# Performance work log

Measured on AMD Instinct MI355X. Metric: run time of the kernel, lower is better.

The kernel has to match this reference:

```python
import jax, jax.numpy as jnp
import numpy as np

NEG_INF = -9e15  # matches torch's -9000000000000000.0 mask value
LEAKY_SLOPE = 0.2  # init alpha


def setup_inputs() -> dict:
    key = jax.random.key(0)
    k1, k2, k3, k4 = jax.random.split(key, 4)
    N, dim = 4096, 128
    hidden = jax.random.normal(k1, (N, dim), dtype=jnp.float32)
    adj = jax.random.randint(k2, (N, N), 0, 5)  # relation codes 0..4
    W = jax.random.normal(k3, (4, dim), dtype=jnp.float32) * (1.0 / np.sqrt(dim))
    b = jax.random.normal(k4, (4,), dtype=jnp.float32) * 0.01
    return {"hidden": hidden, "adj": adj, "W": W, "b": b}


def reference(hidden, adj, W, b):
    # e_k[i,j] = leakyrelu(sum_d h[i,d]*h[j,d]*W[k,d] + b[k])
    # equivalent to the torch repeat/view outer-product + four dim->1 Linears,
    # computed without materializing the [N,N,dim] intermediate.
    hw = hidden[None, :, :] * W[:, None, :]               # [4, N, dim]
    e = jnp.einsum('knd,md->knm', hw, hidden) + b[:, None, None]  # [4, N, N]
    e = jax.nn.leaky_relu(e, negative_slope=LEAKY_SLOPE)
    neg = jnp.asarray(NEG_INF, dtype=e.dtype)
    alpha = jnp.where(adj == 1, e[0], neg)
    alpha = jnp.where(adj == 2, e[1], alpha)
    alpha = jnp.where(adj == 3, e[2], alpha)
    alpha = jnp.where(adj == 4, e[3], alpha)
    alpha = jax.nn.softmax(alpha, axis=-1)                # [N, N]
    return alpha @ hidden                                  # [N, dim]
```

## Files before the change

### kernel.cpp

```cpp
#include <hip/hip_runtime.h>

#define NN 4096
#define DIM 128
#define TN 32
#define TM 64
#define NSPLIT 4
#define NTILES 16

typedef __attribute__((ext_vector_type(8))) short bf16x8;
typedef __attribute__((ext_vector_type(4))) float f32x4;

#define HRS 136
#define HCS 72
#define HROW_USH (TM * HRS)
#define HCOL_USH (128 * HCS)
#define TILE_USH (HROW_USH + HCOL_USH)
#define TILE_CHUNKS 35
#define PST 72

__device__ inline unsigned short f2bf(float x) {
    union { float f; unsigned u; } v; v.f = x;
    unsigned r = v.u + 0x7FFFu + ((v.u >> 16) & 1u);
    return (unsigned short)(r >> 16);
}

__device__ inline void dma16(const void* g, void* l) {
    __builtin_amdgcn_global_load_lds(
        (const __attribute__((address_space(1))) void*)g,
        (__attribute__((address_space(3))) void*)l,
        16, 0, 0);
}

__global__ __launch_bounds__(256) void prep_pack_kernel(
    const float* __restrict__ hidden,
    unsigned short* __restrict__ Hpack)
{
    __shared__ unsigned short T[16][HCS];
    const int tid = threadIdx.x;
    const int t0  = blockIdx.x >> 3;
    const int s   = blockIdx.x & 7;
    const int m0  = t0 * TM;
    unsigned short* rowdst = Hpack + (size_t)t0 * TILE_USH;
    unsigned short* coldst = rowdst + HROW_USH;

    {
        int row = tid >> 5;
        int c4  = (tid & 31) * 4;
        float4 v = *(const float4*)(hidden + (size_t)(m0 + 8 * s + row) * DIM + c4);
        ushort4 o;
        o.x = f2bf(v.x); o.y = f2bf(v.y); o.z = f2bf(v.z); o.w = f2bf(v.w);
        *(ushort4*)(rowdst + (8 * s + row) * HRS + c4) = o;
    }
    {
        int m  = tid >> 2;
        int dc = (tid & 3) * 4;
        float4 v = *(const float4*)(hidden + (size_t)(m0 + m) * DIM + 16 * s + dc);
        T[dc + 0][m] = f2bf(v.x);
        T[dc + 1][m] = f2bf(v.y);
        T[dc + 2][m] = f2bf(v.z);
        T[dc + 3][m] = f2bf(v.w);
    }
    __syncthreads();
    if (tid < 128) {
        int d  = tid >> 3;
        int c8 = (tid & 7) * 8;
        uint4 v = *(const uint4*)(&T[d][c8]);
        *(uint4*)(coldst + (16 * s + d) * HCS + c8) = v;
    }
}

__global__ __launch_bounds__(512)
__attribute__((amdgpu_waves_per_eu(4, 4)))
void gat_flash_kernel(
    const float* __restrict__ hidden,
    const unsigned short* __restrict__ Hpack,
    const int*   __restrict__ adj,
    const float* __restrict__ W,
    const float* __restrict__ bvec,
    float*       __restrict__ Opart,
    float*       __restrict__ lpart)
{
    __shared__ __align__(16) unsigned short HH[2][TILE_USH];
    __shared__ __align__(16) unsigned short Plc[TN * PST];
    __shared__ float redsum[8][16];

    const int tid  = threadIdx.x;
    const int w    = tid >> 6;
    const int lane = tid & 63;
    const int g    = lane >> 4;
    const int l15  = lane & 15;
    const int blk  = blockIdx.x;
    const int nbr  = blk >> 2;
    const int q4   = blk & 3;
    const int n0   = nbr * TN;
    const int gt0  = q4 * NTILES;
    const int rg   = w >> 2;
    const int msw  = w & 3;
    const int lofs = lane * 16;

    const float b0 = bvec[0], b1 = bvec[1], b2 = bvec[2], b3 = bvec[3];

    {
        const char* src = (const char*)(Hpack + (size_t)gt0 * TILE_USH);
        char* dst = (char*)&HH[0][0];
        #pragma unroll
        for (int it = 0; it < 5; ++it) {
            int chunk = it * 8 + w;
            if (chunk < TILE_CHUNKS)
                dma16(src + chunk * 1024 + lofs, dst + chunk * 1024);
        }
    }
    {
        #pragma unroll
        for (int it = 0; it < 2; ++it) {
            int idx = tid + 512 * it;
            int row = idx >> 3;
            int c16 = (idx & 7) * 16;
            int k = row >> 5, r = row & 31;
            const float* hrow = hidden + (size_t)(n0 + r) * DIM + c16;
            const float* wrow = W + k * DIM + c16;
            unsigned short* qdst = &HH[1][row * HRS + c16];
            #pragma unroll
            for (int c = 0; c < 4; ++c) {
                float4 hv = *(const float4*)(hrow + 4 * c);
                float4 wv = *(const float4*)(wrow + 4 * c);
                ushort4 o;
                o.x = f2bf(hv.x * wv.x); o.y = f2bf(hv.y * wv.y);
                o.z = f2bf(hv.z * wv.z); o.w = f2bf(hv.w * wv.w);
                *(ushort4*)(qdst + 4 * c) = o;
            }
        }
    }
    __syncthreads();

    bf16x8 Af[4][4];
    #pragma unroll
    for (int k = 0; k < 4; ++k)
        #pragma unroll
        for (int ks = 0; ks < 4; ++ks)
            Af[k][ks] = *(const bf16x8*)&HH[1][(k * 32 + rg * 16 + l15) * HRS + ks * 32 + 8 * g];
    __syncthreads();

    float lrow[4] = {0.f, 0.f, 0.f, 0.f};
    f32x4 Oacc[2];
    #pragma unroll
    for (int dt = 0; dt < 2; ++dt) Oacc[dt] = (f32x4){0.f, 0.f, 0.f, 0.f};

    const size_t arow = (size_t)(n0 + rg * 16 + 4 * g) * NN;
    int avc[4], avn[4];
    #pragma unroll
    for (int t = 0; t < 4; ++t)
        avc[t] = adj[arow + (size_t)t * NN + gt0 * TM + msw * 16 + l15];

    for (int tile = 0; tile < NTILES; ++tile) {
        const int cur = tile & 1;
        const int nxt = cur ^ 1;

        if (tile + 1 < NTILES) {
            const char* src = (const char*)(Hpack + (size_t)(gt0 + tile + 1) * TILE_USH);
            char* dst = (char*)&HH[nxt][0];
            #pragma unroll
            for (int it = 0; it < 5; ++it) {
                int chunk = it * 8 + w;
                if (chunk < TILE_CHUNKS)
                    dma16(src + chunk * 1024 + lofs, dst + chunk * 1024);
            }
        }

        f32x4 S[4];
        #pragma unroll
        for (int k = 0; k < 4; ++k) S[k] = (f32x4){0.f, 0.f, 0.f, 0.f};
        #pragma unroll
        for (int ks = 0; ks < 4; ++ks) {
            bf16x8 B = *(const bf16x8*)&HH[cur][(msw * 16 + l15) * HRS + ks * 32 + 8 * g];
            #pragma unroll
            for (int k = 0; k < 4; ++k)
                S[k] = __builtin_amdgcn_mfma_f32_16x16x32_bf16(Af[k][ks], B, S[k], 0, 0, 0);
        }

        #pragma unroll
        for (int t = 0; t < 4; ++t) {
            int a = avc[t];
            float s = S[0][t] + b0;
            s = (a == 2) ? S[1][t] + b1 : s;
            s = (a == 3) ? S[2][t] + b2 : s;
            s = (a == 4) ? S[3][t] + b3 : s;
            float e = fmaxf(s, 0.2f * s);
            float p = __expf(e);
            p = (a == 0) ? 0.f : p;
            lrow[t] += p;
            Plc[(rg * 16 + 4 * g + t) * PST + msw * 16 + l15] = f2bf(p);
        }

        if (tile + 1 < NTILES) {
            #pragma unroll
            for (int t = 0; t < 4; ++t)
                avn[t] = adj[arow + (size_t)t * NN + (size_t)(gt0 + tile + 1) * TM + msw * 16 + l15];
        }

        asm volatile("s_waitcnt lgkmcnt(0)\n\ts_barrier" ::: "memory");

        #pragma unroll
        for (int kc = 0; kc < 2; ++kc) {
            bf16x8 Pa = *(const bf16x8*)&Plc[(rg * 16 + l15) * PST + kc * 32 + 8 * g];
            #pragma unroll
            for (int dt = 0; dt < 2; ++dt) {
                bf16x8 Bv = *(const bf16x8*)&HH[cur][HROW_USH + (msw * 32 + dt * 16 + l15) * HCS + kc * 32 + 8 * g];
                Oacc[dt] = __builtin_amdgcn_mfma_f32_16x16x32_bf16(Pa, Bv, Oacc[dt], 0, 0, 0);
            }
        }

        #pragma unroll
        for (int i = 0; i < 4; ++i) avc[i] = avn[i];
        __syncthreads();
    }

    #pragma unroll
    for (int t = 0; t < 4; ++t) {
        float v = lrow[t];
        v += __shfl_xor(v, 1); v += __shfl_xor(v, 2);
        v += __shfl_xor(v, 4); v += __shfl_xor(v, 8);
        if (l15 == 0) redsum[w][4 * g + t] = v;
    }
    __syncthreads();
    if (tid < TN) {
        int rg2 = tid >> 4, rr = tid & 15;
        lpart[blk * TN + tid] = redsum[rg2 * 4 + 0][rr] + redsum[rg2 * 4 + 1][rr]
                              + redsum[rg2 * 4 + 2][rr] + redsum[rg2 * 4 + 3][rr];
    }
    float* Ob = Opart + (size_t)blk * (TN * DIM);
    #pragma unroll
    for (int dt = 0; dt < 2; ++dt)
        #pragma unroll
        for (int t = 0; t < 4; ++t)
            Ob[(rg * 16 + 4 * g + t) * DIM + msw * 32 + dt * 16 + l15] = Oacc[dt][t];
}

__global__ __launch_bounds__(256) void combine_kernel(
    const float* __restrict__ Opart, const float* __restrict__ lpart,
    float* __restrict__ out)
{
    int idx = blockIdx.x * 256 + threadIdx.x;
    int r = idx >> 7, d = idx & 127;
    int nbr = r >> 5, rr = r & 31;
    float O = 0.f, l = 0.f;
    #pragma unroll
    for (int q = 0; q < NSPLIT; ++q) {
        O += Opart[(size_t)(nbr * NSPLIT + q) * (TN * DIM) + rr * 128 + d];
        l += lpart[(nbr * NSPLIT + q) * TN + rr];
    }
    out[idx] = O / l;
}

extern "C" void kernel_launch(void* const* d_in, const int* in_sizes, int n_in,
                              void* d_out, int out_size, void* d_ws, size_t ws_size,
                              hipStream_t stream) {
    const float* hidden = (const float*)d_in[0];
    const int*   adj    = (const int*)d_in[1];
    const float* W      = (const float*)d_in[2];
    const float* b      = (const float*)d_in[3];
    float* out = (float*)d_out;

    char* ws = (char*)d_ws;
    unsigned short* Hpack = (unsigned short*)ws;
    float* Opart = (float*)(ws + (4u << 20));
    float* lpart = (float*)(ws + (12u << 20));

    prep_pack_kernel<<<(NN / TM) * 8, 256, 0, stream>>>(hidden, Hpack);
    gat_flash_kernel<<<512, 512, 0, stream>>>(hidden, Hpack, adj, W, b, Opart, lpart);
    combine_kernel<<<NN * DIM / 256, 256, 0, stream>>>(Opart, lpart, out);
}
```

Before: 133.9 us.

## Give each wave full 16-row strip, split keys 8-way, combine via atomics

Restructures the flash kernel: 256-thread blocks handle 64 query rows, with each wave owning 16 rows across all 64 key columns and all 128 output dims. Per-wave P staging removes the mid-tile block barrier, and Q*W fragments are built directly in registers from global memory. Partial numerators and row sums are accumulated with float atomics into a memset buffer, so the combine kernel becomes a simple divide. This trades more register pressure, atomic traffic and a memset for less synchronisation and a smaller combine step.

```diff
diff --git a/kernel.cpp b/kernel.cpp
--- a/kernel.cpp
+++ b/kernel.cpp
@@ -2,10 +2,10 @@
 
 #define NN 4096
 #define DIM 128
-#define TN 32
+#define TN 64
 #define TM 64
-#define NSPLIT 4
-#define NTILES 16
+#define NSPLIT 8
+#define NTILES 8
 
 typedef __attribute__((ext_vector_type(8))) short bf16x8;
 typedef __attribute__((ext_vector_type(4))) float f32x4;
@@ -69,20 +69,17 @@
     }
 }
 
-__global__ __launch_bounds__(512)
-__attribute__((amdgpu_waves_per_eu(4, 4)))
-void gat_flash_kernel(
+__global__ __launch_bounds__(256, 2) void gat_flash_kernel(
     const float* __restrict__ hidden,
     const unsigned short* __restrict__ Hpack,
     const int*   __restrict__ adj,
     const float* __restrict__ W,
     const float* __restrict__ bvec,
-    float*       __restrict__ Opart,
-    float*       __restrict__ lpart)
+    float*       __restrict__ Onum,
+    float*       __restrict__ lsum)
 {
     __shared__ __align__(16) unsigned short HH[2][TILE_USH];
-    __shared__ __align__(16) unsigned short Plc[TN * PST];
-    __shared__ float redsum[8][16];
+    __shared__ __align__(16) unsigned short Plc[4][16 * PST];
 
     const int tid  = threadIdx.x;
     const int w    = tid >> 6;
@@ -90,12 +87,10 @@
     const int g    = lane >> 4;
     const int l15  = lane & 15;
     const int blk  = blockIdx.x;
-    const int nbr  = blk >> 2;
-    const int q4   = blk & 3;
+    const int nbr  = blk >> 3;
+    const int q8   = blk & 7;
     const int n0   = nbr * TN;
-    const int gt0  = q4 * NTILES;
-    const int rg   = w >> 2;
-    const int msw  = w & 3;
+    const int gt0  = q8 * NTILES;
     const int lofs = lane * 16;
 
     const float b0 = bvec[0], b1 = bvec[1], b2 = bvec[2], b3 = bvec[3];
@@ -104,53 +99,52 @@
         const char* src = (const char*)(Hpack + (size_t)gt0 * TILE_USH);
         char* dst = (char*)&HH[0][0];
         #pragma unroll
-        for (int it = 0; it < 5; ++it) {
-            int chunk = it * 8 + w;
+        for (int it = 0; it < 9; ++it) {
+            int chunk = it * 4 + w;
             if (chunk < TILE_CHUNKS)
                 dma16(src + chunk * 1024 + lofs, dst + chunk * 1024);
         }
     }
-    {
-        #pragma unroll
-        for (int it = 0; it < 2; ++it) {
-            int idx = tid + 512 * it;
-            int row = idx >> 3;
-            int c16 = (idx & 7) * 16;
-            int k = row >> 5, r = row & 31;
-            const float* hrow = hidden + (size_t)(n0 + r) * DIM + c16;
-            const float* wrow = W + k * DIM + c16;
-            unsigned short* qdst = &HH[1][row * HRS + c16];
-            #pragma unroll
-            for (int c = 0; c < 4; ++c) {
-                float4 hv = *(const float4*)(hrow + 4 * c);
-                float4 wv = *(const float4*)(wrow + 4 * c);
-                ushort4 o;
-                o.x = f2bf(hv.x * wv.x); o.y = f2bf(hv.y * wv.y);
-                o.z = f2bf(hv.z * wv.z); o.w = f2bf(hv.w * wv.w);
-                *(ushort4*)(qdst + 4 * c) = o;
-            }
-        }
-    }
+
+    bf16x8 Af[4][4];
+    {
+        const int qrow = n0 + w * 16 + l15;
+        #pragma unroll
+        for (int ks = 0; ks < 4; ++ks) {
+            const float* hp = hidden + (size_t)qrow * DIM + ks * 32 + 8 * g;
+            float4 h0 = *(const float4*)(hp);
+            float4 h1 = *(const float4*)(hp + 4);
+            #pragma unroll
+            for (int k = 0; k < 4; ++k) {
+                const float* wp = W + k * DIM + ks * 32 + 8 * g;
+                float4 w0 = *(const float4*)(wp);
+                float4 w1 = *(const float4*)(wp + 4);
+                bf16x8 a;
+                a[0] = (short)f2bf(h0.x * w0.x); a[1] = (short)f2bf(h0.y * w0.y);
+                a[2] = (short)f2bf(h0.z * w0.z); a[3] = (short)f2bf(h0.w * w0.w);
+                a[4] = (short)f2bf(h1.x * w1.x); a[5] = (short)f2bf(h1.y * w1.y);
+                a[6] = (short)f2bf(h1.z * w1.z); a[7] = (short)f2bf(h1.w * w1.w);
+                Af[k][ks] = a;
+            }
+        }
+    }
+
+    float lrow[4] = {0.f, 0.f, 0.f, 0.f};
+    f32x4 Oacc[8];
+    #pragma unroll
+    for (int dt = 0; dt < 8; ++dt) Oacc[dt] = (f32x4){0.f, 0.f, 0.f, 0.f};
+
+    const size_t arow = (size_t)(n0 + w * 16 + 4 * g) * NN;
+    int avc[16], avn[16];
+    #pragma unroll
+    for (int ch = 0; ch < 4; ++ch)
+        #pragma unroll
+        for (int t = 0; t < 4; ++t)
+            avc[ch * 4 + t] = adj[arow + (size_t)t * NN + gt0 * TM + ch * 16 + l15];
+
     __syncthreads();
 
-    bf16x8 Af[4][4];
-    #pragma unroll
-    for (int k = 0; k < 4; ++k)
-        #pragma unroll
-        for (int ks = 0; ks < 4; ++ks)
-            Af[k][ks] = *(const bf16x8*)&HH[1][(k * 32 + rg * 16 + l15) * HRS + ks * 32 + 8 * g];
-    __syncthreads();
-
-    float lrow[4] = {0.f, 0.f, 0.f, 0.f};
-    f32x4 Oacc[2];
-    #pragma unroll
-    for (int dt = 0; dt < 2; ++dt) Oacc[dt] = (f32x4){0.f, 0.f, 0.f, 0.f};
-
-    const size_t arow = (size_t)(n0 + rg * 16 + 4 * g) * NN;
-    int avc[4], avn[4];
-    #pragma unroll
-    for (int t = 0; t < 4; ++t)
-        avc[t] = adj[arow + (size_t)t * NN + gt0 * TM + msw * 16 + l15];
+    unsigned short* Pw = &Plc[w][0];
 
     for (int tile = 0; tile < NTILES; ++tile) {
         const int cur = tile & 1;
@@ -160,58 +154,60 @@
             const char* src = (const char*)(Hpack + (size_t)(gt0 + tile + 1) * TILE_USH);
             char* dst = (char*)&HH[nxt][0];
             #pragma unroll
-            for (int it = 0; it < 5; ++it) {
-                int chunk = it * 8 + w;
+            for (int it = 0; it < 9; ++it) {
+                int chunk = it * 4 + w;
                 if (chunk < TILE_CHUNKS)
                     dma16(src + chunk * 1024 + lofs, dst + chunk * 1024);
             }
         }
 
-        f32x4 S[4];
-        #pragma unroll
-        for (int k = 0; k < 4; ++k) S[k] = (f32x4){0.f, 0.f, 0.f, 0.f};
-        #pragma unroll
-        for (int ks = 0; ks < 4; ++ks) {
-            bf16x8 B = *(const bf16x8*)&HH[cur][(msw * 16 + l15) * HRS + ks * 32 + 8 * g];
-            #pragma unroll
-            for (int k = 0; k < 4; ++k)
-                S[k] = __builtin_amdgcn_mfma_f32_16x16x32_bf16(Af[k][ks], B, S[k], 0, 0, 0);
-        }
-
-        #pragma unroll
-        for (int t = 0; t < 4; ++t) {
-            int a = avc[t];
-            float s = S[0][t] + b0;
-            s = (a == 2) ? S[1][t] + b1 : s;
-            s = (a == 3) ? S[2][t] + b2 : s;
-            s = (a == 4) ? S[3][t] + b3 : s;
-            float e = fmaxf(s, 0.2f * s);
-            float p = __expf(e);
-            p = (a == 0) ? 0.f : p;
-            lrow[t] += p;
-            Plc[(rg * 16 + 4 * g + t) * PST + msw * 16 + l15] = f2bf(p);
+        #pragma unroll
+        for (int ch = 0; ch < 4; ++ch) {
+            f32x4 S[4];
+            #pragma unroll
+            for (int k = 0; k < 4; ++k) S[k] = (f32x4){0.f, 0.f, 0.f, 0.f};
+            #pragma unroll
+            for (int ks = 0; ks < 4; ++ks) {
+                bf16x8 B = *(const bf16x8*)&HH[cur][(ch * 16 + l15) * HRS + ks * 32 + 8 * g];
+                #pragma unroll
+                for (int k = 0; k < 4; ++k)
+                    S[k] = __builtin_amdgcn_mfma_f32_16x16x32_bf16(Af[k][ks], B, S[k], 0, 0, 0);
+            }
+            #pragma unroll
+            for (int t = 0; t < 4; ++t) {
+                int a = avc[ch * 4 + t];
+                float s = S[0][t] + b0;
+                s = (a == 2) ? S[1][t] + b1 : s;
+                s = (a == 3) ? S[2][t] + b2 : s;
+                s = (a == 4) ? S[3][t] + b3 : s;
+                float e = fmaxf(s, 0.2f * s);
+                float p = __expf(e);
+                p = (a == 0) ? 0.f : p;
+                lrow[t] += p;
+                Pw[(4 * g + t) * PST + ch * 16 + l15] = f2bf(p);
+            }
         }
 
         if (tile + 1 < NTILES) {
             #pragma unroll
-            for (int t = 0; t < 4; ++t)
-                avn[t] = adj[arow + (size_t)t * NN + (size_t)(gt0 + tile + 1) * TM + msw * 16 + l15];
-        }
-
-        asm volatile("s_waitcnt lgkmcnt(0)\n\ts_barrier" ::: "memory");
+            for (int ch = 0; ch < 4; ++ch)
+                #pragma unroll
+                for (int t = 0; t < 4; ++t)
+                    avn[ch * 4 + t] = adj[arow + (size_t)t * NN + (size_t)(gt0 + tile + 1) * TM + ch * 16 + l15];
+        }
 
         #pragma unroll
         for (int kc = 0; kc < 2; ++kc) {
-            bf16x8 Pa = *(const bf16x8*)&Plc[(rg * 16 + l15) * PST + kc * 32 + 8 * g];
-            #pragma unroll
-            for (int dt = 0; dt < 2; ++dt) {
-                bf16x8 Bv = *(const bf16x8*)&HH[cur][HROW_USH + (msw * 32 + dt * 16 + l15) * HCS + kc * 32 + 8 * g];
+            bf16x8 Pa = *(const bf16x8*)&Pw[l15 * PST + kc * 32 + 8 * g];
+            #pragma unroll
+            for (int dt = 0; dt < 8; ++dt) {
+                bf16x8 Bv = *(const bf16x8*)&HH[cur][HROW_USH + (dt * 16 + l15) * HCS + kc * 32 + 8 * g];
                 Oacc[dt] = __builtin_amdgcn_mfma_f32_16x16x32_bf16(Pa, Bv, Oacc[dt], 0, 0, 0);
             }
         }
 
         #pragma unroll
-        for (int i = 0; i < 4; ++i) avc[i] = avn[i];
+        for (int i = 0; i < 16; ++i) avc[i] = avn[i];
         __syncthreads();
     }
 
@@ -220,36 +216,22 @@
         float v = lrow[t];
         v += __shfl_xor(v, 1); v += __shfl_xor(v, 2);
         v += __shfl_xor(v, 4); v += __shfl_xor(v, 8);
-        if (l15 == 0) redsum[w][4 * g + t] = v;
-    }
-    __syncthreads();
-    if (tid < TN) {
-        int rg2 = tid >> 4, rr = tid & 15;
-        lpart[blk * TN + tid] = redsum[rg2 * 4 + 0][rr] + redsum[rg2 * 4 + 1][rr]
-                              + redsum[rg2 * 4 + 2][rr] + redsum[rg2 * 4 + 3][rr];
-    }
-    float* Ob = Opart + (size_t)blk * (TN * DIM);
-    #pragma unroll
-    for (int dt = 0; dt < 2; ++dt)
+        if (l15 == 0) atomicAdd(&lsum[n0 + w * 16 + 4 * g + t], v);
+    }
+    const int orow0 = n0 + w * 16 + 4 * g;
+    #pragma unroll
+    for (int dt = 0; dt < 8; ++dt)
         #pragma unroll
         for (int t = 0; t < 4; ++t)
-            Ob[(rg * 16 + 4 * g + t) * DIM + msw * 32 + dt * 16 + l15] = Oacc[dt][t];
+            atomicAdd(&Onum[(size_t)(orow0 + t) * DIM + dt * 16 + l15], Oacc[dt][t]);
 }
 
 __global__ __launch_bounds__(256) void combine_kernel(
-    const float* __restrict__ Opart, const float* __restrict__ lpart,
+    const float* __restrict__ Onum, const float* __restrict__ lsum,
     float* __restrict__ out)
 {
     int idx = blockIdx.x * 256 + threadIdx.x;
-    int r = idx >> 7, d = idx & 127;
-    int nbr = r >> 5, rr = r & 31;
-    float O = 0.f, l = 0.f;
-    #pragma unroll
-    for (int q = 0; q < NSPLIT; ++q) {
-        O += Opart[(size_t)(nbr * NSPLIT + q) * (TN * DIM) + rr * 128 + d];
-        l += lpart[(nbr * NSPLIT + q) * TN + rr];
-    }
-    out[idx] = O / l;
+    out[idx] = Onum[idx] / lsum[idx >> 7];
 }
 
 extern "C" void kernel_launch(void* const* d_in, const int* in_sizes, int n_in,
@@ -263,10 +245,11 @@
 
     char* ws = (char*)d_ws;
     unsigned short* Hpack = (unsigned short*)ws;
-    float* Opart = (float*)(ws + (4u << 20));
-    float* lpart = (float*)(ws + (12u << 20));
+    float* Onum = (float*)(ws + (4u << 20));
+    float* lsum = (float*)(ws + (6u << 20));
+    hipMemsetAsync(ws + (4u << 20), 0, (size_t)NN * DIM * 4 + (2u << 20) - (size_t)NN * DIM * 4 + NN * 4, stream);
 
     prep_pack_kernel<<<(NN / TM) * 8, 256, 0, stream>>>(hidden, Hpack);
-    gat_flash_kernel<<<512, 512, 0, stream>>>(hidden, Hpack, adj, W, b, Opart, lpart);
-    combine_kernel<<<NN * DIM / 256, 256, 0, stream>>>(Opart, lpart, out);
-}
+    gat_flash_kernel<<<(NN / TN) * NSPLIT, 256, 0, stream>>>(hidden, Hpack, adj, W, b, Onum, lsum);
+    combine_kernel<<<NN * DIM / 256, 256, 0, stream>>>(Onum, lsum, out);
+}
```

After: 130.7 us. -2.4%, faster.
